# Optimization experiments

Hardware: AMD Instinct MI355X
Metric: run time of the kernel (lower is better)

Reference implementation:

```python
import jax, jax.numpy as jnp
import numpy as np

I1, I2, N = 256, 256, 512
B = 2048
FLAT = (I1 + 1) * (I2 + 1)  # 66049


def setup_inputs() -> dict:
    key = jax.random.key(0)
    k1, k2, k3, k4 = jax.random.split(key, 4)
    s1 = 1.0 / np.sqrt(FLAT)
    s2 = 1.0 / np.sqrt(N)
    return {
        "inp1": jax.random.normal(k1, (B, I1), dtype=jnp.float32),
        "inp2": jax.random.normal(k2, (B, I2), dtype=jnp.float32),
        "W1": jax.random.normal(k3, (FLAT, N), dtype=jnp.float32) * s1,
        "b1": jnp.zeros((N,), dtype=jnp.float32),
        "W2": jax.random.normal(k4, (N, N), dtype=jnp.float32) * s2,
        "b2": jnp.zeros((N,), dtype=jnp.float32),
    }


def reference(inp1, inp2, W1, b1, W2, b2):
    b = inp1.shape[0]
    ones = jnp.ones((b, 1), dtype=inp1.dtype)
    a = jnp.concatenate([inp1, ones], axis=-1)  # [B, I1+1]
    c = jnp.concatenate([inp2, ones], axis=-1)  # [B, I2+1]
    # per-sample outer product, flattened: [B, (I1+1)*(I2+1)]
    fusion = jnp.einsum("bi,bj->bij", a, c).reshape(b, -1)
    h = jax.nn.relu(fusion @ W1 + b1)
    return jax.nn.relu(h @ W2 + b2)
```

## Files before the change

kernel.cpp:

```cpp
#include <hip/hip_runtime.h>
#include <hip/hip_bf16.h>
#include <stdint.h>

#define BATCH 2048
#define NHID  512
#define KMAIN 65792
#define NSTEP_ALL 1033
#define AW 320
#define CW 256

typedef __attribute__((ext_vector_type(8))) short short8;
typedef __attribute__((ext_vector_type(4))) short short4v;
typedef __attribute__((ext_vector_type(4))) float f32x4;

#define AS1 __attribute__((address_space(1)))
#define AS3 __attribute__((address_space(3)))

__device__ __forceinline__ unsigned short f2bf(float f) {
    union { float f; unsigned int u; } v; v.f = f;
    unsigned int r = v.u + 0x7FFFu + ((v.u >> 16) & 1u);
    return (unsigned short)(r >> 16);
}
__device__ __forceinline__ float bf2f(unsigned short u) {
    union { unsigned int i; float f; } v; v.i = ((unsigned int)u) << 16;
    return v.f;
}
__device__ __forceinline__ f32x4 MFMA16(short8 a, short8 b, f32x4 c) {
    return __builtin_amdgcn_mfma_f32_16x16x32_bf16(a, b, c, 0, 0, 0);
}

__device__ __forceinline__ int w1_src_row(int k) {
    if (k < KMAIN) return (k >> 8) * 257 + (k & 255);
    int i = k - KMAIN;
    return (i < 257) ? (i * 257 + 256) : -1;
}

__global__ __launch_bounds__(256) void prep_kernel(
        const float* __restrict__ inp1, const float* __restrict__ inp2,
        const float* __restrict__ W1, const float* __restrict__ W2,
        unsigned short* __restrict__ W1f, unsigned short* __restrict__ W2t,
        unsigned short* __restrict__ a_tab, unsigned short* __restrict__ c_tab) {
    __shared__ float T[64][65];
    int b = blockIdx.x;
    int t = threadIdx.x;

    if (b < 8264) {
        int kt = b % 1033, nt = b / 1033;
        int k0 = kt * 64, n0 = nt * 64;
        int nn = t & 63, kk0 = t >> 6;
#pragma unroll
        for (int it = 0; it < 16; ++it) {
            int kk = it * 4 + kk0;
            int row = w1_src_row(k0 + kk);
            T[kk][nn] = (row >= 0) ? W1[(long)row * NHID + n0 + nn] : 0.f;
        }
        __syncthreads();
#pragma unroll
        for (int it = 0; it < 2; ++it) {
            int id = it * 256 + t;
            int n16l = id >> 7;
            int kk   = (id >> 6) & 1;
            int lw   = id & 63;
            short8 o;
#pragma unroll
            for (int e = 0; e < 8; ++e)
                o[e] = (short)f2bf(T[kk * 32 + (lw >> 4) * 8 + e][n16l * 16 + (lw & 15)]);
            size_t off = ((size_t)(((n0 >> 4) + n16l) * NSTEP_ALL + kt) * 2 + kk) * 512
                         + (size_t)lw * 8;
            *reinterpret_cast<short8*>(&W1f[off]) = o;
        }
    } else if (b < 8264 + 64) {
        int bb = b - 8264;
        int kt = bb & 7, nt = bb >> 3;
        int k0 = kt * 64, n0 = nt * 64;
        int nn = t & 63, kk0 = t >> 6;
#pragma unroll
        for (int it = 0; it < 16; ++it) {
            int kk = it * 4 + kk0;
            T[kk][nn] = W2[(long)(k0 + kk) * NHID + n0 + nn];
        }
        __syncthreads();
#pragma unroll
        for (int it = 0; it < 2; ++it) {
            int idx = it * 256 + t;
            int nl = idx >> 3, ch = idx & 7;
            short8 o;
#pragma unroll
            for (int e = 0; e < 8; ++e) o[e] = (short)f2bf(T[ch * 8 + e][nl]);
            *reinterpret_cast<short8*>(&W2t[(long)(n0 + nl) * NHID + k0 + ch * 8]) = o;
        }
    } else {
        int r0 = (b - 8328) * 32;
        for (int idx = t; idx < 32 * (AW / 8); idx += 256) {
            int r = idx / 40, ch = idx - r * 40;
            int m = r0 + r;
            short8 o;
#pragma unroll
            for (int e = 0; e < 8; ++e) {
                int i = ch * 8 + e;
                float v = (i < 256) ? inp1[m * 256 + i] : (i == 256 ? 1.0f : 0.0f);
                o[e] = (short)f2bf(v);
            }
            *reinterpret_cast<short8*>(&a_tab[m * AW + ch * 8]) = o;
        }
        for (int idx = t; idx < 32 * (CW / 8); idx += 256) {
            int r = idx >> 5, ch = idx & 31;
            int m = r0 + r;
            short8 o;
#pragma unroll
            for (int e = 0; e < 8; ++e) o[e] = (short)f2bf(inp2[m * 256 + ch * 8 + e]);
            *reinterpret_cast<short8*>(&c_tab[m * CW + ch * 8]) = o;
        }
    }
}

__device__ __forceinline__ void stage_tile128(const unsigned short* __restrict__ g,
        long row0, long k0, long ld, unsigned short* lds) {
    int t = threadIdx.x;
    int wave = t >> 6, lane = t & 63;
    int rl = lane >> 3;
    int ch = (lane & 7) ^ rl;
    const unsigned short* src0 = g + (row0 + wave * 8 + rl) * ld + k0 + ch * 8;
#pragma unroll
    for (int r = 0; r < 4; ++r) {
        const unsigned short* src = src0 + (long)r * 32 * ld;
        unsigned short* dst = lds + (r * 32 + wave * 8) * 64;
        __builtin_amdgcn_global_load_lds((const AS1 unsigned int*)src,
                                         (AS3 unsigned int*)dst, 16, 0, 0);
    }
}
__device__ __forceinline__ void stage_h_tile(const float* __restrict__ hacc,
        const float* __restrict__ b1, int row0, int k0, unsigned short* lds) {
    int t = threadIdx.x;
    int wave = t >> 6, lane = t & 63;
    int rl = lane >> 3;
    int ch = lane & 7;
    int swch = ch ^ rl;
    f32x4 b0 = *(const f32x4*)(b1 + k0 + ch * 8);
    f32x4 b4 = *(const f32x4*)(b1 + k0 + ch * 8 + 4);
#pragma unroll
    for (int r = 0; r < 4; ++r) {
        int row = r * 32 + wave * 8 + rl;
        const float* src = hacc + (size_t)(row0 + row) * NHID + k0 + ch * 8;
        f32x4 v0 = *(const f32x4*)src;
        f32x4 v4 = *(const f32x4*)(src + 4);
        short8 o;
#pragma unroll
        for (int e = 0; e < 4; ++e) o[e]     = (short)f2bf(fmaxf(v0[e] + b0[e], 0.f));
#pragma unroll
        for (int e = 0; e < 4; ++e) o[4 + e] = (short)f2bf(fmaxf(v4[e] + b4[e], 0.f));
        *reinterpret_cast<short8*>(&lds[row * 64 + swch * 8]) = o;
    }
}
__device__ __forceinline__ short8 read_frag(const unsigned short* lds,
        int rowbase, int kofs, int lane) {
    int row = rowbase + (lane & 15);
    int chunkL = (kofs >> 3) + (lane >> 4);
    int sw = chunkL ^ (row & 7);
    return *reinterpret_cast<const short8*>(&lds[row * 64 + sw * 8]);
}

__global__ __launch_bounds__(256, 2) void gemm1_kernel(
        const unsigned short* __restrict__ a_tab,
        const unsigned short* __restrict__ c_tab,
        const unsigned short* __restrict__ W1f, float* __restrict__ hacc) {
    __shared__ __align__(16) unsigned short a_win[65 * 256];

    int mb = blockIdx.x >> 6;
    int g8 = blockIdx.x & 63;
    int nt = g8 & 15;
    int s  = g8 >> 4;
    int st0 = s * 256;
    int ngroups = (s == 3) ? 65 : 64;

    int lane = threadIdx.x & 63;
    int wv   = threadIdx.x >> 6;
    int rowbase = mb * 256 + wv * 64;
    int frow = lane & 15;
    int kq = (lane >> 4) * 8;
    int r4 = (lane >> 4) * 4;
    int n16a = nt * 2, n16b = nt * 2 + 1;

    short8 cc[4][8];
#pragma unroll
    for (int fm = 0; fm < 4; ++fm)
#pragma unroll
        for (int q = 0; q < 8; ++q)
            cc[fm][q] = *reinterpret_cast<const short8*>(
                &c_tab[(size_t)(rowbase + fm * 16 + frow) * CW + kq + q * 32]);

    {
        const unsigned short* src = a_tab + (size_t)(mb * 256 + threadIdx.x) * AW + s * 64;
        for (int i = 0; i < 65; ++i) a_win[i * 256 + threadIdx.x] = src[i];
    }
    __syncthreads();

    f32x4 acc[4][2];
#pragma unroll
    for (int a = 0; a < 4; ++a)
#pragma unroll
        for (int b2 = 0; b2 < 2; ++b2) acc[a][b2] = (f32x4){0.f, 0.f, 0.f, 0.f};

    short8 bufE0, bufE1, bufE2, bufE3, bufO0, bufO1, bufO2, bufO3;

#define LOADSTEP(st, D) do { \
    const unsigned short* _p0 = W1f + ((size_t)(n16a * NSTEP_ALL + (st))) * 1024 + lane * 8; \
    const unsigned short* _p1 = W1f + ((size_t)(n16b * NSTEP_ALL + (st))) * 1024 + lane * 8; \
    D##0 = *reinterpret_cast<const short8*>(_p0); \
    D##1 = *reinterpret_cast<const short8*>(_p0 + 512); \
    D##2 = *reinterpret_cast<const short8*>(_p1); \
    D##3 = *reinterpret_cast<const short8*>(_p1 + 512); \
} while (0)
#define MFSTEP(B, p) do { \
    _Pragma("unroll") \
    for (int fm = 0; fm < 4; ++fm) { \
        P[fm][0] = MFMA16(cc[fm][2 * (p)],     B##0, P[fm][0]); \
        P[fm][1] = MFMA16(cc[fm][2 * (p)],     B##2, P[fm][1]); \
        P[fm][0] = MFMA16(cc[fm][2 * (p) + 1], B##1, P[fm][0]); \
        P[fm][1] = MFMA16(cc[fm][2 * (p) + 1], B##3, P[fm][1]); \
    } \
} while (0)

    LOADSTEP(st0, bufE);

    for (int g = 0; g < ngroups; ++g) {
        int stg = st0 + g * 4;
        f32x4 P[4][2];
#pragma unroll
        for (int a = 0; a < 4; ++a)
#pragma unroll
            for (int b2 = 0; b2 < 2; ++b2) P[a][b2] = (f32x4){0.f, 0.f, 0.f, 0.f};

        LOADSTEP(stg + 1, bufO);  MFSTEP(bufE, 0);
        LOADSTEP(stg + 2, bufE);  MFSTEP(bufO, 1);
        LOADSTEP(stg + 3, bufO);  MFSTEP(bufE, 2);
        LOADSTEP(stg + 4, bufE);  MFSTEP(bufO, 3);

#pragma unroll
        for (int fm = 0; fm < 4; ++fm) {
            short4v a4 = *reinterpret_cast<const short4v*>(
                &a_win[g * 256 + wv * 64 + fm * 16 + r4]);
#pragma unroll
            for (int r = 0; r < 4; ++r) {
                float av = bf2f((unsigned short)a4[r]);
                acc[fm][0][r] += av * P[fm][0][r];
                acc[fm][1][r] += av * P[fm][1][r];
            }
        }
    }

    if (s == 3) {
#define TAILMF(B, p) do { \
    _Pragma("unroll") \
    for (int fm = 0; fm < 4; ++fm) { \
        const unsigned short* _ar = a_tab + (size_t)(rowbase + fm * 16 + frow) * AW + (p) * 64 + kq; \
        short8 t0 = *reinterpret_cast<const short8*>(_ar); \
        short8 t1 = *reinterpret_cast<const short8*>(_ar + 32); \
        acc[fm][0] = MFMA16(t0, B##0, acc[fm][0]); \
        acc[fm][1] = MFMA16(t0, B##2, acc[fm][1]); \
        acc[fm][0] = MFMA16(t1, B##1, acc[fm][0]); \
        acc[fm][1] = MFMA16(t1, B##3, acc[fm][1]); \
    } \
} while (0)
        LOADSTEP(1029, bufO);  TAILMF(bufE, 0);
        LOADSTEP(1030, bufE);  TAILMF(bufO, 1);
        LOADSTEP(1031, bufO);  TAILMF(bufE, 2);
        LOADSTEP(1032, bufE);  TAILMF(bufO, 3);
        TAILMF(bufE, 4);
    }

#pragma unroll
    for (int fm = 0; fm < 4; ++fm)
#pragma unroll
        for (int fn = 0; fn < 2; ++fn)
#pragma unroll
            for (int r = 0; r < 4; ++r) {
                int row = rowbase + fm * 16 + r4 + r;
                int col = nt * 32 + fn * 16 + frow;
                atomicAdd(&hacc[row * NHID + col], acc[fm][fn][r]);
            }
}

__global__ __launch_bounds__(256) void gemm2_kernel(
        const float* __restrict__ hacc, const float* __restrict__ b1,
        const unsigned short* __restrict__ W2t,
        const float* __restrict__ b2, float* __restrict__ out) {
    __shared__ unsigned short A_s[128 * 64];
    __shared__ unsigned short B_s[128 * 64];
    int m0 = (blockIdx.x >> 2) * 128;
    int n0 = (blockIdx.x & 3) * 128;
    int lane = threadIdx.x & 63;
    int wv = threadIdx.x >> 6;
    int wm = (wv >> 1) * 64;
    int wn = (wv & 1) * 64;

    f32x4 acc[4][4];
#pragma unroll
    for (int a = 0; a < 4; ++a)
#pragma unroll
        for (int b = 0; b < 4; ++b) acc[a][b] = (f32x4){0.f, 0.f, 0.f, 0.f};

    for (int st = 0; st < 8; ++st) {
        int kbase = st * 64;
        __syncthreads();
        stage_tile128(W2t, n0, kbase, NHID, B_s);
        stage_h_tile(hacc, b1, m0, kbase, A_s);
        __syncthreads();
#pragma unroll
        for (int kk = 0; kk < 2; ++kk) {
            short8 aF[4], bF[4];
#pragma unroll
            for (int fm = 0; fm < 4; ++fm) aF[fm] = read_frag(A_s, wm + fm * 16, kk * 32, lane);
#pragma unroll
            for (int fn = 0; fn < 4; ++fn) bF[fn] = read_frag(B_s, wn + fn * 16, kk * 32, lane);
#pragma unroll
            for (int fm = 0; fm < 4; ++fm)
#pragma unroll
                for (int fn = 0; fn < 4; ++fn)
                    acc[fm][fn] = __builtin_amdgcn_mfma_f32_16x16x32_bf16(
                        aF[fm], bF[fn], acc[fm][fn], 0, 0, 0);
        }
    }
    int cl = lane & 15;
    int r4 = (lane >> 4) * 4;
#pragma unroll
    for (int fm = 0; fm < 4; ++fm)
#pragma unroll
        for (int fn = 0; fn < 4; ++fn)
#pragma unroll
            for (int r = 0; r < 4; ++r) {
                int row = m0 + wm + fm * 16 + r4 + r;
                int col = n0 + wn + fn * 16 + cl;
                float x = acc[fm][fn][r] + b2[col];
                out[row * NHID + col] = fmaxf(x, 0.f);
            }
}

extern "C" void kernel_launch(void* const* d_in, const int* in_sizes, int n_in,
                              void* d_out, int out_size, void* d_ws, size_t ws_size,
                              hipStream_t stream) {
    const float* inp1 = (const float*)d_in[0];
    const float* inp2 = (const float*)d_in[1];
    const float* W1   = (const float*)d_in[2];
    const float* b1   = (const float*)d_in[3];
    const float* W2   = (const float*)d_in[4];
    const float* b2   = (const float*)d_in[5];
    float* out = (float*)d_out;

    size_t off = 0;
    auto alloc = [&](size_t bytes) {
        void* p = (char*)d_ws + off;
        off += (bytes + 255) & ~(size_t)255;
        return p;
    };
    unsigned short* W1f   = (unsigned short*)alloc((size_t)32 * NSTEP_ALL * 1024 * 2);
    unsigned short* W2t   = (unsigned short*)alloc((size_t)NHID * NHID * 2);
    float*          hacc  = (float*)alloc((size_t)BATCH * NHID * 4);
    unsigned short* a_tab = (unsigned short*)alloc((size_t)BATCH * AW * 2);
    unsigned short* c_tab = (unsigned short*)alloc((size_t)BATCH * CW * 2);
    (void)ws_size; (void)in_sizes; (void)n_in; (void)out_size;

    hipMemsetAsync(hacc, 0, (size_t)BATCH * NHID * 4, stream);

    prep_kernel<<<8264 + 64 + 64, 256, 0, stream>>>(inp1, inp2, W1, W2,
                                                    W1f, W2t, a_tab, c_tab);

    gemm1_kernel<<<512, 256, 0, stream>>>(a_tab, c_tab, W1f, hacc);
    gemm2_kernel<<<64, 256, 0, stream>>>(hacc, b1, W2t, b2, out);
}
```

Measured before the change: 183.6 us.

## Stage W1 tiles through double-buffered LDS with async global_load_lds

Before, every wave loaded W1 fragments from global memory straight into registers, so the four waves of a block, which share the same W1 columns, each fetched the same data. Now the block cooperatively copies each 4-step group of W1 into a double-buffered LDS area using global_load_lds. The next group is prefetched while the current one feeds the MFMAs, which should cut redundant global traffic and register pressure. In exchange it adds 32KB of LDS per block, which may lower occupancy under launch_bounds(256,2), plus a __syncthreads each group, and the tail now reloads step 1028 explicitly.

Measured after the change: 180.6 us. No clear change (-1.6%).

```diff
diff --git a/kernel.cpp b/kernel.cpp
--- a/kernel.cpp
+++ b/kernel.cpp
@@ -164,6 +164,7 @@
         const unsigned short* __restrict__ a_tab,
         const unsigned short* __restrict__ c_tab,
         const unsigned short* __restrict__ W1f, float* __restrict__ hacc) {
+    __shared__ __align__(16) unsigned short B_s[2][8192];
     __shared__ __align__(16) unsigned short a_win[65 * 256];
 
     int mb = blockIdx.x >> 6;
@@ -193,6 +194,21 @@
         const unsigned short* src = a_tab + (size_t)(mb * 256 + threadIdx.x) * AW + s * 64;
         for (int i = 0; i < 65; ++i) a_win[i * 256 + threadIdx.x] = src[i];
     }
+
+#define STAGE_PHASE(stg, buf) do { \
+    _Pragma("unroll") \
+    for (int j = 0; j < 4; ++j) { \
+        int c = wv * 4 + j;                        \
+        int fnsel = j >> 1, kkc = j & 1; \
+        int n16 = fnsel ? n16b : n16a; \
+        const unsigned short* src = W1f + \
+            ((size_t)(n16 * NSTEP_ALL + (stg) + wv) * 2 + kkc) * 512 + lane * 8; \
+        __builtin_amdgcn_global_load_lds((const AS1 unsigned int*)src, \
+                                         (AS3 unsigned int*)((buf) + c * 512), 16, 0, 0); \
+    } \
+} while (0)
+
+    STAGE_PHASE(st0, &B_s[0][0]);
     __syncthreads();
 
     f32x4 acc[4][2];
@@ -201,8 +217,53 @@
 #pragma unroll
         for (int b2 = 0; b2 < 2; ++b2) acc[a][b2] = (f32x4){0.f, 0.f, 0.f, 0.f};
 
-    short8 bufE0, bufE1, bufE2, bufE3, bufO0, bufO1, bufO2, bufO3;
-
+    int cur = 0;
+    for (int g = 0; g < ngroups; ++g) {
+        int stg = st0 + g * 4;
+        if (g + 1 < ngroups)
+            STAGE_PHASE(stg + 4, &B_s[cur ^ 1][0]);
+        __builtin_amdgcn_sched_barrier(0);
+
+        f32x4 P[4][2];
+#pragma unroll
+        for (int a = 0; a < 4; ++a)
+#pragma unroll
+            for (int b2 = 0; b2 < 2; ++b2) P[a][b2] = (f32x4){0.f, 0.f, 0.f, 0.f};
+
+        const unsigned short* bb = &B_s[cur][0];
+#pragma unroll
+        for (int p = 0; p < 4; ++p) {
+            short8 b00 = *reinterpret_cast<const short8*>(&bb[(p * 4 + 0) * 512 + lane * 8]);
+            short8 b01 = *reinterpret_cast<const short8*>(&bb[(p * 4 + 1) * 512 + lane * 8]);
+            short8 b10 = *reinterpret_cast<const short8*>(&bb[(p * 4 + 2) * 512 + lane * 8]);
+            short8 b11 = *reinterpret_cast<const short8*>(&bb[(p * 4 + 3) * 512 + lane * 8]);
+#pragma unroll
+            for (int fm = 0; fm < 4; ++fm) {
+                P[fm][0] = MFMA16(cc[fm][2 * p],     b00, P[fm][0]);
+                P[fm][1] = MFMA16(cc[fm][2 * p],     b10, P[fm][1]);
+                P[fm][0] = MFMA16(cc[fm][2 * p + 1], b01, P[fm][0]);
+                P[fm][1] = MFMA16(cc[fm][2 * p + 1], b11, P[fm][1]);
+            }
+        }
+
+#pragma unroll
+        for (int fm = 0; fm < 4; ++fm) {
+            short4v a4 = *reinterpret_cast<const short4v*>(
+                &a_win[g * 256 + wv * 64 + fm * 16 + r4]);
+#pragma unroll
+            for (int r = 0; r < 4; ++r) {
+                float av = bf2f((unsigned short)a4[r]);
+                acc[fm][0][r] += av * P[fm][0][r];
+                acc[fm][1][r] += av * P[fm][1][r];
+            }
+        }
+
+        __syncthreads();
+        cur ^= 1;
+    }
+
+    if (s == 3) {
+        short8 bufE0, bufE1, bufE2, bufE3, bufO0, bufO1, bufO2, bufO3;
 #define LOADSTEP(st, D) do { \
     const unsigned short* _p0 = W1f + ((size_t)(n16a * NSTEP_ALL + (st))) * 1024 + lane * 8; \
     const unsigned short* _p1 = W1f + ((size_t)(n16b * NSTEP_ALL + (st))) * 1024 + lane * 8; \
@@ -211,45 +272,6 @@
     D##2 = *reinterpret_cast<const short8*>(_p1); \
     D##3 = *reinterpret_cast<const short8*>(_p1 + 512); \
 } while (0)
-#define MFSTEP(B, p) do { \
-    _Pragma("unroll") \
-    for (int fm = 0; fm < 4; ++fm) { \
-        P[fm][0] = MFMA16(cc[fm][2 * (p)],     B##0, P[fm][0]); \
-        P[fm][1] = MFMA16(cc[fm][2 * (p)],     B##2, P[fm][1]); \
-        P[fm][0] = MFMA16(cc[fm][2 * (p) + 1], B##1, P[fm][0]); \
-        P[fm][1] = MFMA16(cc[fm][2 * (p) + 1], B##3, P[fm][1]); \
-    } \
-} while (0)
-
-    LOADSTEP(st0, bufE);
-
-    for (int g = 0; g < ngroups; ++g) {
-        int stg = st0 + g * 4;
-        f32x4 P[4][2];
-#pragma unroll
-        for (int a = 0; a < 4; ++a)
-#pragma unroll
-            for (int b2 = 0; b2 < 2; ++b2) P[a][b2] = (f32x4){0.f, 0.f, 0.f, 0.f};
-
-        LOADSTEP(stg + 1, bufO);  MFSTEP(bufE, 0);
-        LOADSTEP(stg + 2, bufE);  MFSTEP(bufO, 1);
-        LOADSTEP(stg + 3, bufO);  MFSTEP(bufE, 2);
-        LOADSTEP(stg + 4, bufE);  MFSTEP(bufO, 3);
-
-#pragma unroll
-        for (int fm = 0; fm < 4; ++fm) {
-            short4v a4 = *reinterpret_cast<const short4v*>(
-                &a_win[g * 256 + wv * 64 + fm * 16 + r4]);
-#pragma unroll
-            for (int r = 0; r < 4; ++r) {
-                float av = bf2f((unsigned short)a4[r]);
-                acc[fm][0][r] += av * P[fm][0][r];
-                acc[fm][1][r] += av * P[fm][1][r];
-            }
-        }
-    }
-
-    if (s == 3) {
 #define TAILMF(B, p) do { \
     _Pragma("unroll") \
     for (int fm = 0; fm < 4; ++fm) { \
@@ -262,6 +284,7 @@
         acc[fm][1] = MFMA16(t1, B##3, acc[fm][1]); \
     } \
 } while (0)
+        LOADSTEP(1028, bufE);
         LOADSTEP(1029, bufO);  TAILMF(bufE, 0);
         LOADSTEP(1030, bufE);  TAILMF(bufO, 1);
         LOADSTEP(1031, bufO);  TAILMF(bufE, 2);
```
